# Performance work log

Hardware: AMD Instinct MI355X
Metric: run time of the kernel (lower is better)

Reference implementation:

```python
import jax, jax.numpy as jnp
import numpy as np


def setup_inputs() -> dict:
    key = jax.random.key(0)
    ks = jax.random.split(key, 8)
    B, W, H, C = 4, 64, 64, 256
    C2 = C // 2
    s = 0.05
    x = jax.random.normal(ks[0], (B, W, H, C), dtype=jnp.float32)
    Wq = jax.random.normal(ks[1], (C, C2), dtype=jnp.float32) * s
    bq = jax.random.normal(ks[2], (C2,), dtype=jnp.float32) * s
    Wk = jax.random.normal(ks[3], (C, C2), dtype=jnp.float32) * s
    bk = jax.random.normal(ks[4], (C2,), dtype=jnp.float32) * s
    Wv = jax.random.normal(ks[5], (C, C), dtype=jnp.float32) * s
    bv = jax.random.normal(ks[6], (C,), dtype=jnp.float32) * s
    # gamma is initialized to 0 in the original; use a nonzero value so the
    # attention branch actually contributes (math is identical).
    gamma = jnp.array([0.5], dtype=jnp.float32)
    return {"x": x, "Wq": Wq, "bq": bq, "Wk": Wk, "bk": bk, "Wv": Wv, "bv": bv, "gamma": gamma}


def reference(x, Wq, bq, Wk, bk, Wv, bv, gamma):
    B, W, H, C = x.shape
    N = W * H
    # 1x1 convs == per-pixel linear projections
    q = jnp.einsum('bwhc,cd->bwhd', x, Wq) + bq   # [B,W,H,C/2]
    k = jnp.einsum('bwhc,cd->bwhd', x, Wk) + bk   # [B,W,H,C/2]
    v = jnp.einsum('bwhc,cd->bwhd', x, Wv) + bv   # [B,W,H,C]
    # Faithful to original: raw row-major reshape (B,W,H,Cq) -> (B,Cq,N)
    # (this mixes spatial and channel axes, exactly as the TF code does)
    pq = q.reshape(B, -1, N)                      # [B,C/2,N]
    pk = k.reshape(B, -1, N)                      # [B,C/2,N]
    pv = v.reshape(B, -1, N)                      # [B,C,N]
    energy = jnp.einsum('bcn,bcm->bnm', pq, pk)   # [B,N,N] (pq transposed)
    attention = jax.nn.softmax(energy, axis=-1)   # [B,N,N]
    out = jnp.einsum('bcm,bnm->bcn', pv, attention)  # pv @ attention^T
    out = out.reshape(B, W, H, C)
    return gamma * out + x
```

## Files before the change

### kernel.cpp

```cpp
#include <hip/hip_runtime.h>
#include <stdint.h>


typedef __attribute__((ext_vector_type(8)))  short short8;
typedef __attribute__((ext_vector_type(4)))  float f32x4;
typedef __attribute__((ext_vector_type(16))) float f32x16;
typedef __attribute__((ext_vector_type(4)))  unsigned short u16x4;

#define MFMA16 __builtin_amdgcn_mfma_f32_16x16x32_bf16
#define MFMA32 __builtin_amdgcn_mfma_f32_32x32x16_bf16

__device__ __forceinline__ unsigned short f2bf(float f) {
    union { float f; uint32_t u; } v; v.f = f;
    uint32_t r = (v.u + 0x7FFFu + ((v.u >> 16) & 1u)) >> 16;
    return (unsigned short)r;
}
__device__ __forceinline__ float bf2f(unsigned short h) {
    union { uint32_t u; float f; } v; v.u = ((uint32_t)h) << 16;
    return v.f;
}

__global__ void prep_w(const float* __restrict__ Wq, const float* __restrict__ bq,
                       const float* __restrict__ Wk, const float* __restrict__ bk,
                       const float* __restrict__ Wv, const float* __restrict__ bv,
                       unsigned short* __restrict__ Wt, float* __restrict__ bias) {
    int g = blockIdx.x * 256 + threadIdx.x;
    int c = g & 255, d = g >> 8;
    float val;
    if (d < 128)      val = Wq[c * 128 + d];
    else if (d < 256) val = Wk[c * 128 + (d - 128)];
    else              val = Wv[c * 256 + (d - 256)];
    Wt[d * 256 + c] = f2bf(val);
    if (g < 512) {
        float bb;
        if (g < 128)      bb = bq[g];
        else if (g < 256) bb = bk[g - 128];
        else              bb = bv[g - 256];
        bias[g] = bb;
    }
}

__global__ __launch_bounds__(256) void proj(
        const float* __restrict__ x, const unsigned short* __restrict__ Wt,
        const float* __restrict__ bias,
        unsigned short* __restrict__ Qrm, unsigned short* __restrict__ Krm,
        unsigned short* __restrict__ Vbf) {
    __shared__ unsigned short T[128 * 136];
    int bid = blockIdx.x;
    int tid = threadIdx.x;
    int wave = tid >> 6, lane = tid & 63;
    int l16 = lane & 15, quad = lane >> 4;

    int kind, b, a, vh = 0;
    if (bid < 256) { kind = bid >> 7; int s = bid & 127; b = s >> 5; a = s & 31; }
    else           { kind = 2; int s = bid - 256; vh = s >> 7; b = (s >> 5) & 3; a = s & 31; }

    short8 af[2][8];
    #pragma unroll
    for (int g = 0; g < 2; ++g) {
        int p_local = wave * 32 + g * 16 + l16;
        int pix = (kind == 2) ? (b * 4096 + a * 128 + p_local)
                              : (b * 4096 + a + 32 * p_local);
        const float* xr = x + (size_t)pix * 256;
        #pragma unroll
        for (int kk = 0; kk < 8; ++kk) {
            f32x4 u0 = *(const f32x4*)(xr + kk * 32 + quad * 8);
            f32x4 u1 = *(const f32x4*)(xr + kk * 32 + quad * 8 + 4);
            short8 h;
            h[0] = (short)f2bf(u0[0]); h[1] = (short)f2bf(u0[1]);
            h[2] = (short)f2bf(u0[2]); h[3] = (short)f2bf(u0[3]);
            h[4] = (short)f2bf(u1[0]); h[5] = (short)f2bf(u1[1]);
            h[6] = (short)f2bf(u1[2]); h[7] = (short)f2bf(u1[3]);
            af[g][kk] = h;
        }
    }

    if (kind < 2) {
        int dbase = kind * 128;
        unsigned short* out = kind ? Krm : Qrm;
        #pragma unroll 1
        for (int dt = 0; dt < 8; ++dt) {
            int d = dbase + dt * 16 + l16;
            float bval = bias[d];
            f32x4 acc0 = {0.f,0.f,0.f,0.f}, acc1 = {0.f,0.f,0.f,0.f};
            #pragma unroll
            for (int kk = 0; kk < 8; ++kk) {
                short8 wrow = *(const short8*)(Wt + d * 256 + kk * 32 + quad * 8);
                acc0 = MFMA16(af[0][kk], wrow, acc0, 0, 0, 0);
                acc1 = MFMA16(af[1][kk], wrow, acc1, 0, 0, 0);
            }
            #pragma unroll
            for (int g = 0; g < 2; ++g) {
                f32x4 acc = g ? acc1 : acc0;
                u16x4 pk;
                #pragma unroll
                for (int reg = 0; reg < 4; ++reg) pk[reg] = f2bf(acc[reg] + bval);
                *(u16x4*)(T + (dt * 16 + l16) * 136 + wave * 32 + g * 16 + quad * 4) = pk;
            }
        }
        __syncthreads();
        unsigned short* ob = out + (b << 19) + a * 128 * 128;
        #pragma unroll
        for (int it = 0; it < 8; ++it) {
            int ci = it * 256 + tid;
            int row = ci >> 4, cj = ci & 15;
            *(short8*)(ob + row * 128 + cj * 8) = *(const short8*)(T + row * 136 + cj * 8);
        }
    } else {
        #pragma unroll 1
        for (int dt = 0; dt < 8; ++dt) {
            int d = 256 + vh * 128 + dt * 16 + l16;
            f32x4 acc0 = {0.f,0.f,0.f,0.f}, acc1 = {0.f,0.f,0.f,0.f};
            #pragma unroll
            for (int kk = 0; kk < 8; ++kk) {
                short8 wrow = *(const short8*)(Wt + d * 256 + kk * 32 + quad * 8);
                acc0 = MFMA16(wrow, af[0][kk], acc0, 0, 0, 0);
                acc1 = MFMA16(wrow, af[1][kk], acc1, 0, 0, 0);
            }
            int dvl = dt * 16 + quad * 4;
            f32x4 bv4 = *(const f32x4*)(bias + 256 + vh * 128 + dvl);
            #pragma unroll
            for (int g = 0; g < 2; ++g) {
                f32x4 acc = g ? acc1 : acc0;
                u16x4 pk;
                #pragma unroll
                for (int reg = 0; reg < 4; ++reg) pk[reg] = f2bf(acc[reg] + bv4[reg]);
                int p_local = wave * 32 + g * 16 + l16;
                *(u16x4*)(T + p_local * 136 + dvl) = pk;
            }
        }
        __syncthreads();
        #pragma unroll
        for (int it = 0; it < 8; ++it) {
            int cid = it * 256 + tid;
            int c_local = cid >> 8, w = cid & 255;
            int p_local = c_local * 16 + (w >> 4);
            int m = (w >> 4) * 256 + vh * 128 + (w & 15) * 8;
            *(short8*)(Vbf + (b << 20) + (size_t)(a * 8 + c_local) * 4096 + m)
                = *(const short8*)(T + p_local * 136 + (w & 15) * 8);
        }
    }
}

__global__ __launch_bounds__(256, 2) void attn(
        const unsigned short* __restrict__ Qrm, const unsigned short* __restrict__ Krm,
        const unsigned short* __restrict__ Vbf, unsigned short* __restrict__ Opart,
        float* __restrict__ Lpart) {
    __shared__ unsigned short Vs[256 * 72];
    __shared__ unsigned short Ps[64 * 72];

    int bid = blockIdx.x;
    int comb = bid & 7, qt = bid >> 3;
    int b = comb >> 1, ks = comb & 1;
    int tid = threadIdx.x, wave = tid >> 6, lane = tid & 63;
    int l32 = lane & 31, half = lane >> 5;
    int mt = wave & 1, nt = wave >> 1;

    const unsigned short* Qb = Qrm + (b << 19);
    const unsigned short* Kb = Krm + (b << 19);
    const unsigned short* Vb = Vbf + (b << 20);

    int q0 = qt * 64;

    short8 qf[8];
    {
        const unsigned short* qrow = Qb + (q0 + nt * 32 + l32) * 128 + half * 8;
        #pragma unroll
        for (int kk = 0; kk < 8; ++kk) qf[kk] = *(const short8*)(qrow + kk * 16);
    }

    f32x16 O[2][2];
    #pragma unroll
    for (int i = 0; i < 2; ++i)
        #pragma unroll
        for (int j = 0; j < 2; ++j)
            #pragma unroll
            for (int r = 0; r < 16; ++r) O[i][j][r] = 0.f;
    float l_run = 0.f;

    const int m_base = ks * 2048;
    int vrow = tid >> 3, vch = tid & 7;

    short8 vreg[8];
    #pragma unroll
    for (int i = 0; i < 8; ++i)
        vreg[i] = *(const short8*)(Vb + (size_t)(vrow + i * 32) * 4096 + m_base + vch * 8);
    short8 kf[8];
    {
        const unsigned short* krow = Kb + (m_base + mt * 32 + l32) * 128 + half * 8;
        #pragma unroll
        for (int kk = 0; kk < 8; ++kk) kf[kk] = *(const short8*)(krow + kk * 16);
    }

    #pragma unroll 1
    for (int kt = 0; kt < 32; ++kt) {
        __syncthreads();
        #pragma unroll
        for (int i = 0; i < 8; ++i)
            *(short8*)(Vs + (vrow + i * 32) * 72 + vch * 8) = vreg[i];

        f32x16 S;
        #pragma unroll
        for (int r = 0; r < 16; ++r) S[r] = 0.f;
        #pragma unroll
        for (int kk = 0; kk < 8; ++kk) S = MFMA32(kf[kk], qf[kk], S, 0, 0, 0);

        float rs = 0.f;
        #pragma unroll
        for (int g = 0; g < 4; ++g) {
            u16x4 pk;
            #pragma unroll
            for (int i = 0; i < 4; ++i) {
                float p = __expf(S[g * 4 + i]);
                rs += p;
                pk[i] = f2bf(p);
            }
            *(u16x4*)(Ps + (nt * 32 + l32) * 72 + mt * 32 + g * 8 + half * 4) = pk;
        }
        rs += __shfl_xor(rs, 32);
        l_run += rs;

        __syncthreads();

        if (kt < 31) {
            int m1 = m_base + (kt + 1) * 64;
            #pragma unroll
            for (int i = 0; i < 8; ++i)
                vreg[i] = *(const short8*)(Vb + (size_t)(vrow + i * 32) * 4096 + m1 + vch * 8);
            const unsigned short* krow = Kb + (m1 + mt * 32 + l32) * 128 + half * 8;
            #pragma unroll
            for (int kk = 0; kk < 8; ++kk) kf[kk] = *(const short8*)(krow + kk * 16);
        }

        #pragma unroll
        for (int k2 = 0; k2 < 4; ++k2) {
            short8 pa0 = *(const short8*)(Ps + (l32) * 72 + k2 * 16 + half * 8);
            short8 pa1 = *(const short8*)(Ps + (32 + l32) * 72 + k2 * 16 + half * 8);
            #pragma unroll
            for (int c2 = 0; c2 < 2; ++c2) {
                short8 vb = *(const short8*)(Vs + ((wave * 2 + c2) * 32 + l32) * 72 + k2 * 16 + half * 8);
                O[0][c2] = MFMA32(pa0, vb, O[0][c2], 0, 0, 0);
                O[1][c2] = MFMA32(pa1, vb, O[1][c2], 0, 0, 0);
            }
        }
    }

    unsigned short* Op = Opart + ((size_t)(ks * 4 + b) << 20);
    #pragma unroll
    for (int q2 = 0; q2 < 2; ++q2)
        #pragma unroll
        for (int c2 = 0; c2 < 2; ++c2) {
            int c = (wave * 2 + c2) * 32 + l32;
            #pragma unroll
            for (int r = 0; r < 16; ++r) {
                int n = q0 + q2 * 32 + (r & 3) + 8 * (r >> 2) + 4 * half;
                Op[(size_t)n * 256 + c] = f2bf(O[q2][c2][r]);
            }
        }
    if (half == 0) {
        int n = q0 + nt * 32 + l32;
        Lpart[((ks * 2 + mt) * 4 + b) * 4096 + n] = l_run;
    }
}

__global__ __launch_bounds__(256) void merge_out(
        const unsigned short* __restrict__ Opart, const float* __restrict__ Lpart,
        const float* __restrict__ x, const float* __restrict__ gamma,
        float* __restrict__ out) {
    __shared__ float tile[64][65];
    __shared__ float wsm[64];
    int b  = blockIdx.x >> 6;
    int n0 = (blockIdx.x & 63) << 6;
    int tid = threadIdx.x;
    float g = gamma[0];
    if (tid < 64) {
        int n = n0 + tid;
        float L = 0.f;
        #pragma unroll
        for (int s = 0; s < 4; ++s) L += Lpart[(s * 4 + b) * 4096 + n];
        wsm[tid] = g / L;
    }
    __syncthreads();
    int cl  = tid & 63, nl4 = tid >> 6;
    int nl  = tid & 63, cl4 = tid >> 6;
    for (int cc = 0; cc < 4; ++cc) {
        for (int i = 0; i < 16; ++i) {
            int n = n0 + i * 4 + nl4;
            int c = (cc << 6) + cl;
            float On = 0.f;
            #pragma unroll
            for (int s = 0; s < 2; ++s)
                On += bf2f(Opart[((size_t)(s * 4 + b) << 20) + (size_t)n * 256 + c]);
            tile[cl][i * 4 + nl4] = On * wsm[i * 4 + nl4];
        }
        __syncthreads();
        for (int j = 0; j < 16; ++j) {
            int c = (cc << 6) + j * 4 + cl4;
            int idx = (b << 20) + c * 4096 + n0 + nl;
            out[idx] = tile[j * 4 + cl4][nl] + x[idx];
        }
        __syncthreads();
    }
}

extern "C" void kernel_launch(void* const* d_in, const int* in_sizes, int n_in,
                              void* d_out, int out_size, void* d_ws, size_t ws_size,
                              hipStream_t stream) {
    const float* x     = (const float*)d_in[0];
    const float* Wq    = (const float*)d_in[1];
    const float* bq    = (const float*)d_in[2];
    const float* Wk    = (const float*)d_in[3];
    const float* bk    = (const float*)d_in[4];
    const float* Wv    = (const float*)d_in[5];
    const float* bv    = (const float*)d_in[6];
    const float* gamma = (const float*)d_in[7];
    float* out = (float*)d_out;

    if (ws_size < 34080768u) return;

    char* ws = (char*)d_ws;
    unsigned short* Wt    = (unsigned short*)(ws);
    float*          bias  = (float*)        (ws +   262144);
    unsigned short* Qrm   = (unsigned short*)(ws +   264192);
    unsigned short* Krm   = (unsigned short*)(ws +  4458496);
    unsigned short* Vbf   = (unsigned short*)(ws +  8652800);
    unsigned short* Opart = (unsigned short*)(ws + 17041408);
    float*          Lpart = (float*)        (ws + 33818624);

    prep_w   <<<512, 256, 0, stream>>>(Wq, bq, Wk, bk, Wv, bv, Wt, bias);
    proj     <<<512, 256, 0, stream>>>(x, Wt, bias, Qrm, Krm, Vbf);
    attn     <<<512, 256, 0, stream>>>(Qrm, Krm, Vbf, Opart, Lpart);
    merge_out<<<256, 256, 0, stream>>>(Opart, Lpart, x, gamma, out);
}
```

Before: 192.2 us.

## Load V fragments directly into registers and double-buffer P to drop a barrier

V tiles are no longer staged through shared memory. Each wave loads its own MFMA B-operand fragments straight from global memory into registers, and the next tile is prefetched after the PV MFMAs. The P buffer in shared memory is double-buffered by iteration parity, which allows the leading __syncthreads per iteration to be removed. This cuts LDS traffic, LDS footprint and one barrier per tile. In exchange, the global loads of V become strided per lane (32 rows at a 4096 stride), and the V prefetch is issued later, with less time to hide its latency.

```diff
diff --git a/kernel.cpp b/kernel.cpp
--- a/kernel.cpp
+++ b/kernel.cpp
@@ -146,8 +146,7 @@
         const unsigned short* __restrict__ Qrm, const unsigned short* __restrict__ Krm,
         const unsigned short* __restrict__ Vbf, unsigned short* __restrict__ Opart,
         float* __restrict__ Lpart) {
-    __shared__ unsigned short Vs[256 * 72];
-    __shared__ unsigned short Ps[64 * 72];
+    __shared__ unsigned short Ps[2 * 64 * 72];
 
     int bid = blockIdx.x;
     int comb = bid & 7, qt = bid >> 3;
@@ -179,25 +178,25 @@
     float l_run = 0.f;
 
     const int m_base = ks * 2048;
-    int vrow = tid >> 3, vch = tid & 7;
-
-    short8 vreg[8];
-    #pragma unroll
-    for (int i = 0; i < 8; ++i)
-        vreg[i] = *(const short8*)(Vb + (size_t)(vrow + i * 32) * 4096 + m_base + vch * 8);
+
     short8 kf[8];
     {
         const unsigned short* krow = Kb + (m_base + mt * 32 + l32) * 128 + half * 8;
         #pragma unroll
         for (int kk = 0; kk < 8; ++kk) kf[kk] = *(const short8*)(krow + kk * 16);
     }
+    short8 vreg[2][4];
+    #pragma unroll
+    for (int c2 = 0; c2 < 2; ++c2)
+        #pragma unroll
+        for (int k2 = 0; k2 < 4; ++k2)
+            vreg[c2][k2] = *(const short8*)(Vb + (size_t)((wave * 2 + c2) * 32 + l32) * 4096
+                                            + m_base + k2 * 16 + half * 8);
 
     #pragma unroll 1
     for (int kt = 0; kt < 32; ++kt) {
-        __syncthreads();
-        #pragma unroll
-        for (int i = 0; i < 8; ++i)
-            *(short8*)(Vs + (vrow + i * 32) * 72 + vch * 8) = vreg[i];
+        int m0 = m_base + kt * 64;
+        unsigned short* Pb = Ps + (kt & 1) * (64 * 72);
 
         f32x16 S;
         #pragma unroll
@@ -215,7 +214,7 @@
                 rs += p;
                 pk[i] = f2bf(p);
             }
-            *(u16x4*)(Ps + (nt * 32 + l32) * 72 + mt * 32 + g * 8 + half * 4) = pk;
+            *(u16x4*)(Pb + (nt * 32 + l32) * 72 + mt * 32 + g * 8 + half * 4) = pk;
         }
         rs += __shfl_xor(rs, 32);
         l_run += rs;
@@ -223,25 +222,29 @@
         __syncthreads();
 
         if (kt < 31) {
-            int m1 = m_base + (kt + 1) * 64;
-            #pragma unroll
-            for (int i = 0; i < 8; ++i)
-                vreg[i] = *(const short8*)(Vb + (size_t)(vrow + i * 32) * 4096 + m1 + vch * 8);
-            const unsigned short* krow = Kb + (m1 + mt * 32 + l32) * 128 + half * 8;
+            const unsigned short* krow = Kb + (m0 + 64 + mt * 32 + l32) * 128 + half * 8;
             #pragma unroll
             for (int kk = 0; kk < 8; ++kk) kf[kk] = *(const short8*)(krow + kk * 16);
         }
 
         #pragma unroll
         for (int k2 = 0; k2 < 4; ++k2) {
-            short8 pa0 = *(const short8*)(Ps + (l32) * 72 + k2 * 16 + half * 8);
-            short8 pa1 = *(const short8*)(Ps + (32 + l32) * 72 + k2 * 16 + half * 8);
-            #pragma unroll
-            for (int c2 = 0; c2 < 2; ++c2) {
-                short8 vb = *(const short8*)(Vs + ((wave * 2 + c2) * 32 + l32) * 72 + k2 * 16 + half * 8);
-                O[0][c2] = MFMA32(pa0, vb, O[0][c2], 0, 0, 0);
-                O[1][c2] = MFMA32(pa1, vb, O[1][c2], 0, 0, 0);
-            }
+            short8 pa0 = *(const short8*)(Pb + (l32) * 72 + k2 * 16 + half * 8);
+            short8 pa1 = *(const short8*)(Pb + (32 + l32) * 72 + k2 * 16 + half * 8);
+            O[0][0] = MFMA32(pa0, vreg[0][k2], O[0][0], 0, 0, 0);
+            O[0][1] = MFMA32(pa0, vreg[1][k2], O[0][1], 0, 0, 0);
+            O[1][0] = MFMA32(pa1, vreg[0][k2], O[1][0], 0, 0, 0);
+            O[1][1] = MFMA32(pa1, vreg[1][k2], O[1][1], 0, 0, 0);
+        }
+
+        if (kt < 31) {
+            int m1 = m0 + 64;
+            #pragma unroll
+            for (int c2 = 0; c2 < 2; ++c2)
+                #pragma unroll
+                for (int k2 = 0; k2 < 4; ++k2)
+                    vreg[c2][k2] = *(const short8*)(Vb + (size_t)((wave * 2 + c2) * 32 + l32) * 4096
+                                                    + m1 + k2 * 16 + half * 8);
         }
     }
 
```

New measurement: 231.7 us. 20.5% more time.
